# Performance work log

Hardware: AMD Instinct MI355X
Metric: run time of the kernel (lower is better)

The kernel has to match this reference:

```python
import jax, jax.numpy as jnp
import numpy as np

NH = 64
KS = 3
H_DIM = 32
IN_DIM = 1

# U-Net conv shapes, matching get_indices(unet_nh=64)
KERN_SHAPES = ([(NH, 2, KS, KS)] + [(NH, NH, KS, KS)] * 7
               + [(NH, 2 * NH, KS, KS), (NH, NH, KS, KS)] * 3
               + [(2, NH, 1, 1)])
BIAS_SHAPES = [(NH,)] * 14 + [(2,)]
KERN_SIZES = [int(np.prod(s)) for s in KERN_SHAPES]
BIAS_SIZES = [int(np.prod(s)) for s in BIAS_SHAPES]
OUT_DIM = sum(KERN_SIZES) + sum(BIAS_SIZES)  # 592002


def hypernet(hp, W1, b1, W2, b2, Wo, bo):
    # hp: [B, in_dim] -> per-sample flat weight vector [B, OUT_DIM]
    h = hp @ W1.T + b1          # no activation between lin1/lin2 (as in source)
    h = h @ W2.T + b2
    w = jnp.tanh(h @ Wo.T + bo)
    wl, bl = [], []
    off = 0
    for s, n in zip(KERN_SHAPES, KERN_SIZES):
        wl.append(w[:, off:off + n].reshape(-1, *s)); off += n
    for s, n in zip(BIAS_SHAPES, BIAS_SIZES):
        bl.append(w[:, off:off + n].reshape(-1, *s)); off += n
    return wl, bl, w


def bconv(x, w, b, pad):
    # per-sample conv: x [B,C,H,W], w [B,O,C,k,k], b [B,O]
    def one(xi, wi, bi):
        y = jax.lax.conv_general_dilated(xi[None], wi, (1, 1), [(pad, pad), (pad, pad)])
        return y[0] + bi[:, None, None]
    return jax.vmap(one)(x, w, b)


def maxpool2(x):
    B, C, H, W = x.shape
    return x.reshape(B, C, H // 2, 2, W // 2, 2).max(axis=(3, 5))


def up2_ac(x):
    # bilinear upsample scale=2, align_corners=True
    B, C, H, W = x.shape
    Ho, Wo = 2 * H, 2 * W
    ys = (jnp.arange(Ho, dtype=jnp.float32) * (H - 1) / (Ho - 1))
    y0 = jnp.floor(ys).astype(jnp.int32); y1 = jnp.minimum(y0 + 1, H - 1)
    wy = (ys - y0.astype(jnp.float32))[None, None, :, None]
    xs = (jnp.arange(Wo, dtype=jnp.float32) * (W - 1) / (Wo - 1))
    x0 = jnp.floor(xs).astype(jnp.int32); x1 = jnp.minimum(x0 + 1, W - 1)
    wx = (xs - x0.astype(jnp.float32))[None, None, None, :]
    r = x[:, :, y0, :] * (1 - wy) + x[:, :, y1, :] * wy
    return r[:, :, :, x0] * (1 - wx) + r[:, :, :, x1] * wx


def setup_inputs() -> dict:
    key = jax.random.key(0)
    ks = jax.random.split(key, 9)
    B, H, W = 8, 256, 256
    s1 = 1.0 / (IN_DIM * NH) ** 0.5
    s2 = 1.0 / (H_DIM * NH) ** 0.5
    return {
        "zf": jax.random.normal(ks[0], (B, H, W, 2), jnp.float32),
        "y": jax.random.normal(ks[1], (B, H, W, 2), jnp.float32),
        "hyperparams": jax.random.uniform(ks[2], (B, IN_DIM), jnp.float32),
        "W1": jax.random.normal(ks[3], (H_DIM, IN_DIM), jnp.float32) * s1,
        "b1": jax.random.normal(ks[4], (H_DIM,), jnp.float32) * s1,
        "W2": jax.random.normal(ks[5], (H_DIM, H_DIM), jnp.float32) * s2,
        "b2": jax.random.normal(ks[6], (H_DIM,), jnp.float32) * s2,
        "Wo": jax.random.normal(ks[7], (OUT_DIM, H_DIM), jnp.float32) * s2,
        "bo": jax.random.normal(ks[8], (OUT_DIM,), jnp.float32) * s2,
    }


def reference(zf, y, hyperparams, W1, b1, W2, b2, Wo, bo):
    wl, bl, flat = hypernet(hyperparams, W1, b1, W2, b2, Wo, bo)
    # l1 over all generated weights+biases == sum |flat| per sample
    l1_weights = jnp.sum(jnp.abs(flat), axis=1)
    relu = jax.nn.relu
    x = jnp.transpose(zf, (0, 3, 1, 2))  # [B,2,H,W]
    x = relu(bconv(x, wl[0], bl[0], 1))
    conv1 = relu(bconv(x, wl[1], bl[1], 1))
    x = maxpool2(conv1)
    x = relu(bconv(x, wl[2], bl[2], 1))
    conv2 = relu(bconv(x, wl[3], bl[3], 1))
    x = maxpool2(conv2)
    x = relu(bconv(x, wl[4], bl[4], 1))
    conv3 = relu(bconv(x, wl[5], bl[5], 1))
    x = maxpool2(conv3)
    x = relu(bconv(x, wl[6], bl[6], 1))
    conv4 = relu(bconv(x, wl[7], bl[7], 1))
    x = jnp.concatenate([up2_ac(conv4), conv3], axis=1)
    x = relu(bconv(x, wl[8], bl[8], 1))
    x = relu(bconv(x, wl[9], bl[9], 1))
    x = jnp.concatenate([up2_ac(x), conv2], axis=1)
    x = relu(bconv(x, wl[10], bl[10], 1))
    x = relu(bconv(x, wl[11], bl[11], 1))
    x = jnp.concatenate([up2_ac(x), conv1], axis=1)
    x = relu(bconv(x, wl[12], bl[12], 1))
    x = relu(bconv(x, wl[13], bl[13], 1))
    x = bconv(x, wl[14], bl[14], 0)  # 1x1 conv, padding=0
    x = jnp.transpose(x, (0, 2, 3, 1))
    x = zf + x  # residual=True
    return (x, l1_weights)
```

## Files before the change

kernel.cpp:

```cpp
#include <hip/hip_runtime.h>
#include <hip/hip_bf16.h>
#include <math.h>

#define ODIM 592002L
#define WRB  589824L
#define NB 8

typedef __hip_bfloat16 bf16;
typedef __bf16  bf16x8 __attribute__((ext_vector_type(8)));
typedef float   f32x16 __attribute__((ext_vector_type(16)));
typedef short   s16x8  __attribute__((ext_vector_type(8)));

__device__ __forceinline__ float b2f(bf16 x) { return __bfloat162float(x); }
__device__ __forceinline__ bf16 f2b(float x) { return __float2bfloat16(x); }
__device__ __forceinline__ bf16x8 bzero() { return __builtin_bit_cast(bf16x8, (s16x8)0); }

__global__ __launch_bounds__(256) void hyper_h(
    const float* __restrict__ hp, const float* __restrict__ W1,
    const float* __restrict__ b1, const float* __restrict__ W2,
    const float* __restrict__ b2, float* __restrict__ h2out)
{
    __shared__ float h1[NB][32];
    int t = threadIdx.x;
    int b = t >> 5, i = t & 31;
    h1[b][i] = hp[b] * W1[i] + b1[i];
    __syncthreads();
    float acc = b2[i];
    #pragma unroll
    for (int j = 0; j < 32; ++j) acc += h1[b][j] * W2[i * 32 + j];
    h2out[b * 32 + i] = acc;
}

__global__ __launch_bounds__(256) void genw(
    const float* __restrict__ Wo, const float* __restrict__ bo,
    const float* __restrict__ h2, bf16* __restrict__ wfb,
    float* __restrict__ part)
{
    __shared__ float h2s[256];
    __shared__ float red[256];
    int t = threadIdx.x;
    h2s[t] = h2[t];
    __syncthreads();
    long o = (long)blockIdx.x * 256 + t;
    float absacc[NB];
    #pragma unroll
    for (int b = 0; b < NB; ++b) absacc[b] = 0.f;
    if (o < ODIM) {
        float row[32];
        const float4* wp = (const float4*)(Wo + o * 32);
        #pragma unroll
        for (int q = 0; q < 8; ++q) {
            float4 v = wp[q];
            row[q*4+0] = v.x; row[q*4+1] = v.y; row[q*4+2] = v.z; row[q*4+3] = v.w;
        }
        float bias = bo[o];
        #pragma unroll
        for (int b = 0; b < NB; ++b) {
            float acc = bias;
            #pragma unroll
            for (int k = 0; k < 32; ++k) acc += h2s[b*32+k] * row[k];
            float w = tanhf(acc);
            wfb[(long)b * ODIM + o] = f2b(w);
            absacc[b] = fabsf(w);
        }
    }
    for (int b = 0; b < NB; ++b) {
        red[t] = absacc[b];
        __syncthreads();
        for (int s = 128; s > 0; s >>= 1) {
            if (t < s) red[t] += red[t + s];
            __syncthreads();
        }
        if (t == 0) part[(long)blockIdx.x * NB + b] = red[0];
        __syncthreads();
    }
}

__global__ __launch_bounds__(256) void l1_reduce(
    const float* __restrict__ part, int nblk, float* __restrict__ outp)
{
    __shared__ float red[256];
    int t = threadIdx.x; int b = t & 7, ch = t >> 3;
    float s = 0.f;
    for (int i = ch; i < nblk; i += 32) s += part[(long)i * 8 + b];
    red[t] = s;
    __syncthreads();
    for (int st = 128; st >= 8; st >>= 1) {
        if (t < st) red[t] += red[t + st];
        __syncthreads();
    }
    if (t < 8) outp[t] = red[t];
}

__global__ __launch_bounds__(256) void repack(
    const bf16* __restrict__ wfb, bf16* __restrict__ wr,
    int koff, int Cinfull, long roff, int K)
{
    int i = blockIdx.x * 256 + threadIdx.x;
    int b = blockIdx.y;
    if (i >= 64 * K) return;
    int fid = i >> 9;
    int lane = (i >> 3) & 63;
    int j = i & 7;
    int h = fid & 1;
    int kk = fid >> 1;
    int k4 = kk & 3;
    int tapq = kk >> 2;
    int tap = tapq % 9;
    int pass = tapq / 9;
    int oc = h * 32 + (lane & 31);
    int icf = pass * 64 + k4 * 16 + (lane >> 5) * 8 + j;
    wr[(long)b * WRB + roff + i] =
        wfb[(long)b * ODIM + koff + ((long)oc * Cinfull + icf) * 9 + tap];
}

template<int TR, int TC, int MODE>
__device__ __forceinline__ void stage_tile(
    const bf16* __restrict__ src, int Hc, int Wc, int y0, int x0,
    bf16* lin, int t)
{
    const int XL = TC + 2;
    const int total = (TR + 2) * XL * 8;
    for (int idx = t; idx < total; idx += 256) {
        const int g = idx & 7;
        const int rem = idx >> 3;
        const int xl = rem % XL;
        const int gy = y0 + rem / XL - 1, gx = x0 + xl - 1;
        bf16x8 v = bzero();
        if ((unsigned)gy < (unsigned)Hc && (unsigned)gx < (unsigned)Wc) {
            if constexpr (MODE == 0) {
                v = *(const bf16x8*)(src + (((long)gy * Wc) + gx) * 64 + g * 8);
            } else if constexpr (MODE == 1) {
                const int Ws = Wc * 2;
                const bf16* p = src + (((long)(gy*2) * Ws) + gx*2) * 64 + g * 8;
                bf16x8 aa = *(const bf16x8*)p;
                bf16x8 bb = *(const bf16x8*)(p + 64);
                bf16x8 cc = *(const bf16x8*)(p + (long)Ws * 64);
                bf16x8 dd = *(const bf16x8*)(p + (long)Ws * 64 + 64);
                #pragma unroll
                for (int j = 0; j < 8; ++j) {
                    float m = fmaxf(fmaxf((float)aa[j], (float)bb[j]),
                                    fmaxf((float)cc[j], (float)dd[j]));
                    v[j] = (__bf16)m;
                }
            } else {
                const int Hs = Hc >> 1, Ws = Wc >> 1;
                const float sy = (float)(Hs - 1) / (float)(Hc - 1);
                const float sx = (float)(Ws - 1) / (float)(Wc - 1);
                float ys = gy * sy, xs = gx * sx;
                int yy0 = (int)ys, xx0 = (int)xs;
                int yy1 = min(yy0 + 1, Hs - 1), xx1 = min(xx0 + 1, Ws - 1);
                float wy = ys - (float)yy0, wx = xs - (float)xx0;
                bf16x8 q00 = *(const bf16x8*)(src + ((long)yy0*Ws + xx0)*64 + g*8);
                bf16x8 q01 = *(const bf16x8*)(src + ((long)yy0*Ws + xx1)*64 + g*8);
                bf16x8 q10 = *(const bf16x8*)(src + ((long)yy1*Ws + xx0)*64 + g*8);
                bf16x8 q11 = *(const bf16x8*)(src + ((long)yy1*Ws + xx1)*64 + g*8);
                #pragma unroll
                for (int j = 0; j < 8; ++j) {
                    float r0 = (float)q00[j]*(1.f-wx) + (float)q01[j]*wx;
                    float r1 = (float)q10[j]*(1.f-wx) + (float)q11[j]*wx;
                    v[j] = (__bf16)(r0*(1.f-wy) + r1*wy);
                }
            }
        }
        long byte = (((long)rem) * 128 + g * 16) ^ ((xl & 7) << 4);
        *(bf16x8*)((char*)lin + byte) = v;
    }
}

template<int MODE>
__global__ __launch_bounds__(256, 3) void conv_mfma(
    const bf16* __restrict__ src1, const bf16* __restrict__ src2,
    int Hc, int Wc,
    const bf16* __restrict__ wr, long roff,
    const bf16* __restrict__ wfb, int boff,
    bf16* __restrict__ outp)
{
    const int TR = 8, TC = 32, XL = TC + 2;
    __shared__ bf16 lin[(TR + 2) * XL * 64];
    __shared__ float biasf[64];
    const int t = threadIdx.x;
    const int lane = t & 63;
    const int w = t >> 6;
    const int b = blockIdx.z;
    const int y0 = blockIdx.y * TR;
    const int x0 = blockIdx.x * TC;
    const int lx = lane & 31;

    f32x16 acc00 = {}, acc01 = {}, acc10 = {}, acc11 = {};

    const bf16* wl = wr + (long)b * WRB + roff;
    const long bb = (long)b * ODIM + boff;
    if (t < 64) biasf[t] = b2f(wfb[bb + t]);

    int xl128[3], swz[3];
    #pragma unroll
    for (int d = 0; d < 3; ++d) {
        int xl = lx + d;
        xl128[d] = xl * 128;
        swz[d] = (xl & 7) << 4;
    }
    const int icbl = (lane >> 5) * 16;

    auto kpass = [&](int p) {
        #pragma unroll
        for (int tap = 0; tap < 9; ++tap) {
            const int dy = tap / 3, dxi = tap % 3;
            const int rb0 = (w + dy) * (XL * 128);
            const int rb1 = (w + 4 + dy) * (XL * 128);
            bf16x8 af[4][2];
            #pragma unroll
            for (int k4 = 0; k4 < 4; ++k4) {
                const int fid = ((p * 9 + tap) * 4 + k4) * 2;
                const bf16* pk = wl + ((long)fid << 9) + (lane << 3);
                af[k4][0] = *(const bf16x8*)pk;
                af[k4][1] = *(const bf16x8*)(pk + 512);
            }
            #pragma unroll
            for (int k4 = 0; k4 < 4; ++k4) {
                const int co = xl128[dxi] + ((k4 * 32 + icbl) ^ swz[dxi]);
                bf16x8 b0 = *(const bf16x8*)((const char*)lin + rb0 + co);
                bf16x8 b1 = *(const bf16x8*)((const char*)lin + rb1 + co);
                acc00 = __builtin_amdgcn_mfma_f32_32x32x16_bf16(af[k4][0], b0, acc00, 0, 0, 0);
                acc01 = __builtin_amdgcn_mfma_f32_32x32x16_bf16(af[k4][1], b0, acc01, 0, 0, 0);
                acc10 = __builtin_amdgcn_mfma_f32_32x32x16_bf16(af[k4][0], b1, acc10, 0, 0, 0);
                acc11 = __builtin_amdgcn_mfma_f32_32x32x16_bf16(af[k4][1], b1, acc11, 0, 0, 0);
            }
        }
    };

    stage_tile<TR, TC, MODE>(src1, Hc, Wc, y0, x0, lin, t);
    __syncthreads();
    kpass(0);
    if (src2) {
        __syncthreads();
        stage_tile<TR, TC, 0>(src2, Hc, Wc, y0, x0, lin, t);
        __syncthreads();
        kpass(1);
    }

    __syncthreads();
    #pragma unroll
    for (int half = 0; half < 2; ++half) {
        const int r = w + half * 4;
        const int pixidx = r * TC + lx;
        const int psw = (pixidx & 7) << 4;
        #pragma unroll
        for (int ocs = 0; ocs < 2; ++ocs) {
            const f32x16& A = half ? (ocs ? acc11 : acc10) : (ocs ? acc01 : acc00);
            #pragma unroll
            for (int q = 0; q < 4; ++q) {
                const int oc0 = ocs * 32 + 8 * q + 4 * (lane >> 5);
                ushort4 pk;
                float v0 = fmaxf(A[4*q+0] + biasf[oc0 + 0], 0.f);
                float v1 = fmaxf(A[4*q+1] + biasf[oc0 + 1], 0.f);
                float v2 = fmaxf(A[4*q+2] + biasf[oc0 + 2], 0.f);
                float v3 = fmaxf(A[4*q+3] + biasf[oc0 + 3], 0.f);
                pk.x = __builtin_bit_cast(unsigned short, f2b(v0));
                pk.y = __builtin_bit_cast(unsigned short, f2b(v1));
                pk.z = __builtin_bit_cast(unsigned short, f2b(v2));
                pk.w = __builtin_bit_cast(unsigned short, f2b(v3));
                long byte = ((long)pixidx * 128 + oc0 * 2) ^ psw;
                *(ushort4*)((char*)lin + byte) = pk;
            }
        }
    }
    __syncthreads();
    bf16* outt = outp + (((long)b * Hc + y0) * Wc + x0) * 64;
    #pragma unroll
    for (int off = t * 16; off < TR * TC * 128; off += 4096) {
        int pix = off >> 7;
        int r = pix >> 5, c = pix & 31;
        long sb = (long)off ^ ((pix & 7) << 4);
        bf16x8 v = *(const bf16x8*)((const char*)lin + sb);
        *(bf16x8*)((char*)outt + ((long)(r * Wc + c)) * 128 + (off & 127)) = v;
    }
}

__global__ __launch_bounds__(256) void conv0_k(
    const float* __restrict__ zf, const bf16* __restrict__ wfb,
    bf16* __restrict__ outp)
{
    __shared__ float wsh[2][9][64];
    __shared__ float bsh[64];
    const int t = threadIdx.x;
    const int b = blockIdx.z;
    const long wb = (long)b * ODIM;
    for (int i = t; i < 1152; i += 256) {
        int oc = i / 18, r2 = i % 18, ic = r2 / 9, tap = r2 % 9;
        wsh[ic][tap][oc] = b2f(wfb[wb + i]);
    }
    if (t < 64) bsh[t] = b2f(wfb[wb + 591104 + t]);
    __syncthreads();
    const int pl = t >> 3, g = t & 7;
    const int pix = blockIdx.x * 32 + pl;
    const int y = pix >> 8, x = pix & 255;
    float acc[8];
    #pragma unroll
    for (int j = 0; j < 8; ++j) acc[j] = bsh[g * 8 + j];
    const float* zb = zf + (long)b * 131072;
    #pragma unroll
    for (int dy = 0; dy < 3; ++dy) {
        int yy = y + dy - 1;
        if ((unsigned)yy >= 256u) continue;
        #pragma unroll
        for (int dx = 0; dx < 3; ++dx) {
            int xx = x + dx - 1;
            if ((unsigned)xx >= 256u) continue;
            const float* p = zb + ((long)yy * 256 + xx) * 2;
            float v0 = p[0], v1 = p[1];
            int tap = dy * 3 + dx;
            #pragma unroll
            for (int j = 0; j < 8; ++j)
                acc[j] += v0 * wsh[0][tap][g*8+j] + v1 * wsh[1][tap][g*8+j];
        }
    }
    bf16x8 v;
    #pragma unroll
    for (int j = 0; j < 8; ++j) v[j] = (__bf16)fmaxf(acc[j], 0.f);
    *(bf16x8*)(outp + ((long)b * 65536 + pix) * 64 + g * 8) = v;
}

__global__ __launch_bounds__(256) void final_k(
    const bf16* __restrict__ X, const bf16* __restrict__ wfb,
    const float* __restrict__ zf, float* __restrict__ outp)
{
    __shared__ float wsh[128];
    __shared__ float bsh[2];
    const int t = threadIdx.x;
    const int i = blockIdx.x * 256 + t;
    const int pix = i & 65535;
    const int b = i >> 16;
    const long wb = (long)b * ODIM;
    if (t < 128) wsh[t] = b2f(wfb[wb + 590976 + t]);
    if (t < 2) bsh[t] = b2f(wfb[wb + 592000 + t]);
    __syncthreads();
    const bf16* p = X + ((long)b * 65536 + pix) * 64;
    float a0 = bsh[0], a1 = bsh[1];
    #pragma unroll
    for (int gq = 0; gq < 8; ++gq) {
        bf16x8 v = *(const bf16x8*)(p + gq * 8);
        #pragma unroll
        for (int j = 0; j < 8; ++j) {
            float f = (float)v[j];
            a0 += f * wsh[gq*8 + j];
            a1 += f * wsh[64 + gq*8 + j];
        }
    }
    long zi = ((long)b * 65536 + pix) * 2;
    outp[zi] = zf[zi] + a0;
    outp[zi + 1] = zf[zi + 1] + a1;
}

extern "C" void kernel_launch(void* const* d_in, const int* in_sizes, int n_in,
                              void* d_out, int out_size, void* d_ws, size_t ws_size,
                              hipStream_t stream)
{
    (void)in_sizes; (void)n_in; (void)out_size; (void)ws_size;
    const float* zf = (const float*)d_in[0];
    const float* hp = (const float*)d_in[2];
    const float* W1 = (const float*)d_in[3];
    const float* b1 = (const float*)d_in[4];
    const float* W2 = (const float*)d_in[5];
    const float* b2 = (const float*)d_in[6];
    const float* Wo = (const float*)d_in[7];
    const float* bo = (const float*)d_in[8];
    float* out = (float*)d_out;

    char* base = (char*)d_ws;
    float* h2   = (float*)base;  base += 1024;
    float* part = (float*)base;  base += 18504L * 4 + 32;
    bf16* wfb   = (bf16*)base;   base += 4736016L * 2 + 32;
    bf16* WREP  = (bf16*)base;   base += 4718592L * 2;
    bf16* Y256  = (bf16*)base;   base += 33554432L * 2;
    bf16* C1s   = (bf16*)base;   base += 33554432L * 2;
    bf16* D128a = (bf16*)base;   base += 8388608L * 2;
    bf16* C2s   = (bf16*)base;   base += 8388608L * 2;
    bf16* X128  = (bf16*)base;   base += 8388608L * 2;
    bf16* E64a  = (bf16*)base;   base += 2097152L * 2;
    bf16* C3s   = (bf16*)base;   base += 2097152L * 2;
    bf16* X64   = (bf16*)base;   base += 2097152L * 2;
    bf16* F32a  = (bf16*)base;   base += 524288L * 2;
    bf16* C4    = (bf16*)base;   base += 524288L * 2;

    hyper_h<<<1, 256, 0, stream>>>(hp, W1, b1, W2, b2, h2);
    const int ngb = (int)((ODIM + 255) / 256);
    genw<<<ngb, 256, 0, stream>>>(Wo, bo, h2, wfb, part);
    l1_reduce<<<1, 256, 0, stream>>>(part, ngb, out + 1048576);

    const int K1=1152, K2=38016, K3=74880, K4=111744, K5=148608,
              K6=185472, K7=222336, K8=259200, K9=332928, K10=369792,
              K11=443520, K12=480384, K13=554112;
    const int BB = 591104;
    const long R1=0, R2=36864, R3=73728, R4=110592, R5=147456, R6=184320,
               R7=221184, R8=258048, R9=331776, R10=368640, R11=442368,
               R12=479232, R13=552960;

    repack<<<dim3(144, 8), 256, 0, stream>>>(wfb, WREP, K1, 64, R1, 576);
    repack<<<dim3(144, 8), 256, 0, stream>>>(wfb, WREP, K2, 64, R2, 576);
    repack<<<dim3(144, 8), 256, 0, stream>>>(wfb, WREP, K3, 64, R3, 576);
    repack<<<dim3(144, 8), 256, 0, stream>>>(wfb, WREP, K4, 64, R4, 576);
    repack<<<dim3(144, 8), 256, 0, stream>>>(wfb, WREP, K5, 64, R5, 576);
    repack<<<dim3(144, 8), 256, 0, stream>>>(wfb, WREP, K6, 64, R6, 576);
    repack<<<dim3(144, 8), 256, 0, stream>>>(wfb, WREP, K7, 64, R7, 576);
    repack<<<dim3(288, 8), 256, 0, stream>>>(wfb, WREP, K8, 128, R8, 1152);
    repack<<<dim3(144, 8), 256, 0, stream>>>(wfb, WREP, K9, 64, R9, 576);
    repack<<<dim3(288, 8), 256, 0, stream>>>(wfb, WREP, K10, 128, R10, 1152);
    repack<<<dim3(144, 8), 256, 0, stream>>>(wfb, WREP, K11, 64, R11, 576);
    repack<<<dim3(288, 8), 256, 0, stream>>>(wfb, WREP, K12, 128, R12, 1152);
    repack<<<dim3(144, 8), 256, 0, stream>>>(wfb, WREP, K13, 64, R13, 576);

    conv0_k<<<dim3(2048, 1, 8), 256, 0, stream>>>(zf, wfb, Y256);

    conv_mfma<0><<<dim3(8,32,8),  256, 0, stream>>>(Y256, nullptr, 256,256, WREP, R1,  wfb, BB+64,  C1s);
    conv_mfma<1><<<dim3(4,16,8),  256, 0, stream>>>(C1s,  nullptr, 128,128, WREP, R2,  wfb, BB+128, D128a);
    conv_mfma<0><<<dim3(4,16,8),  256, 0, stream>>>(D128a,nullptr, 128,128, WREP, R3,  wfb, BB+192, C2s);
    conv_mfma<1><<<dim3(2,8,8),   256, 0, stream>>>(C2s,  nullptr, 64,64,   WREP, R4,  wfb, BB+256, E64a);
    conv_mfma<0><<<dim3(2,8,8),   256, 0, stream>>>(E64a, nullptr, 64,64,   WREP, R5,  wfb, BB+320, C3s);
    conv_mfma<1><<<dim3(1,4,8),   256, 0, stream>>>(C3s,  nullptr, 32,32,   WREP, R6,  wfb, BB+384, F32a);
    conv_mfma<0><<<dim3(1,4,8),   256, 0, stream>>>(F32a, nullptr, 32,32,   WREP, R7,  wfb, BB+448, C4);
    conv_mfma<2><<<dim3(2,8,8),   256, 0, stream>>>(C4,   C3s, 64,64,   WREP, R8,  wfb, BB+512, E64a);
    conv_mfma<0><<<dim3(2,8,8),   256, 0, stream>>>(E64a, nullptr, 64,64, WREP, R9,  wfb, BB+576, X64);
    conv_mfma<2><<<dim3(4,16,8),  256, 0, stream>>>(X64,  C2s, 128,128, WREP, R10, wfb, BB+640, D128a);
    conv_mfma<0><<<dim3(4,16,8),  256, 0, stream>>>(D128a,nullptr,128,128, WREP, R11, wfb, BB+704, X128);
    conv_mfma<2><<<dim3(8,32,8),  256, 0, stream>>>(X128, C1s, 256,256, WREP, R12, wfb, BB+768, Y256);
    conv_mfma<0><<<dim3(8,32,8),  256, 0, stream>>>(Y256, nullptr,256,256, WREP, R13, wfb, BB+832, C1s);

    final_k<<<dim3(2048), 256, 0, stream>>>(C1s, wfb, zf, out);
}
```

Baseline: 629.7 us.

## Enlarge conv tiles to 16 rows with register row reuse; merge repack launches

The MFMA conv kernel now processes 16-row tiles. Each wave owns 4 consecutive output rows and keeps 6 input rows of LDS fragments in registers, so the three dy taps reuse loaded B fragments and each weight fragment feeds 8 MFMAs instead of 4. Occupancy in launch bounds drops from 3 to 2 blocks per CU to fit the larger accumulator and fragment state, and the grids are halved, which leaves fewer blocks on the small layers. The 13 weight-repack launches are merged into one kernel that selects each layer's offsets by index range.

```diff
diff --git a/kernel.cpp b/kernel.cpp
--- a/kernel.cpp
+++ b/kernel.cpp
@@ -92,16 +92,32 @@
     if (t < 8) outp[t] = red[t];
 }
 
-__global__ __launch_bounds__(256) void repack(
-    const bf16* __restrict__ wfb, bf16* __restrict__ wr,
-    int koff, int Cinfull, long roff, int K)
+__global__ __launch_bounds__(256) void repack_all(
+    const bf16* __restrict__ wfb, bf16* __restrict__ wr)
 {
     int i = blockIdx.x * 256 + threadIdx.x;
     int b = blockIdx.y;
-    if (i >= 64 * K) return;
-    int fid = i >> 9;
-    int lane = (i >> 3) & 63;
-    int j = i & 7;
+    if (i >= (int)WRB) return;
+    int roff, koff, dual = 0;
+    if      (i < 36864)  { roff = 0;      koff = 1152;  }
+    else if (i < 73728)  { roff = 36864;  koff = 38016; }
+    else if (i < 110592) { roff = 73728;  koff = 74880; }
+    else if (i < 147456) { roff = 110592; koff = 111744;}
+    else if (i < 184320) { roff = 147456; koff = 148608;}
+    else if (i < 221184) { roff = 184320; koff = 185472;}
+    else if (i < 258048) { roff = 221184; koff = 222336;}
+    else if (i < 331776) { roff = 258048; koff = 259200; dual = 1; }
+    else if (i < 368640) { roff = 331776; koff = 332928;}
+    else if (i < 442368) { roff = 368640; koff = 369792; dual = 1; }
+    else if (i < 479232) { roff = 442368; koff = 443520;}
+    else if (i < 552960) { roff = 479232; koff = 480384; dual = 1; }
+    else                 { roff = 552960; koff = 554112;}
+    int li = i - roff;
+    int K = dual ? 1152 : 576;
+    int Cinfull = dual ? 128 : 64;
+    int fid = li >> 9;
+    int lane = (li >> 3) & 63;
+    int j = li & 7;
     int h = fid & 1;
     int kk = fid >> 1;
     int k4 = kk & 3;
@@ -110,7 +126,8 @@
     int pass = tapq / 9;
     int oc = h * 32 + (lane & 31);
     int icf = pass * 64 + k4 * 16 + (lane >> 5) * 8 + j;
-    wr[(long)b * WRB + roff + i] =
+    (void)K;
+    wr[(long)b * WRB + i] =
         wfb[(long)b * ODIM + koff + ((long)oc * Cinfull + icf) * 9 + tap];
 }
 
@@ -169,14 +186,14 @@
 }
 
 template<int MODE>
-__global__ __launch_bounds__(256, 3) void conv_mfma(
+__global__ __launch_bounds__(256, 2) void conv_mfma(
     const bf16* __restrict__ src1, const bf16* __restrict__ src2,
     int Hc, int Wc,
     const bf16* __restrict__ wr, long roff,
     const bf16* __restrict__ wfb, int boff,
     bf16* __restrict__ outp)
 {
-    const int TR = 8, TC = 32, XL = TC + 2;
+    const int TR = 16, TC = 32, XL = TC + 2;
     __shared__ bf16 lin[(TR + 2) * XL * 64];
     __shared__ float biasf[64];
     const int t = threadIdx.x;
@@ -187,44 +204,59 @@
     const int x0 = blockIdx.x * TC;
     const int lx = lane & 31;
 
-    f32x16 acc00 = {}, acc01 = {}, acc10 = {}, acc11 = {};
+    f32x16 acc[4][2];
+    #pragma unroll
+    for (int r = 0; r < 4; ++r) {
+        acc[r][0] = {}; acc[r][1] = {};
+    }
 
     const bf16* wl = wr + (long)b * WRB + roff;
-    const long bb = (long)b * ODIM + boff;
-    if (t < 64) biasf[t] = b2f(wfb[bb + t]);
-
-    int xl128[3], swz[3];
+    if (t < 64) biasf[t] = b2f(wfb[(long)b * ODIM + boff + t]);
+
+    int cofs[3], swz[3];
     #pragma unroll
     for (int d = 0; d < 3; ++d) {
         int xl = lx + d;
-        xl128[d] = xl * 128;
+        cofs[d] = xl * 128;
         swz[d] = (xl & 7) << 4;
     }
     const int icbl = (lane >> 5) * 16;
+    const int wrow = 4 * w;
 
     auto kpass = [&](int p) {
         #pragma unroll
-        for (int tap = 0; tap < 9; ++tap) {
-            const int dy = tap / 3, dxi = tap % 3;
-            const int rb0 = (w + dy) * (XL * 128);
-            const int rb1 = (w + 4 + dy) * (XL * 128);
-            bf16x8 af[4][2];
+        for (int k4 = 0; k4 < 4; ++k4) {
+            const int cb = k4 * 32 + icbl;
+            bf16x8 bf[6][3];
             #pragma unroll
-            for (int k4 = 0; k4 < 4; ++k4) {
-                const int fid = ((p * 9 + tap) * 4 + k4) * 2;
-                const bf16* pk = wl + ((long)fid << 9) + (lane << 3);
-                af[k4][0] = *(const bf16x8*)pk;
-                af[k4][1] = *(const bf16x8*)(pk + 512);
+            for (int rr = 0; rr < 4; ++rr) {
+                const int rb = (wrow + rr) * (XL * 128);
+                #pragma unroll
+                for (int d = 0; d < 3; ++d)
+                    bf[rr][d] = *(const bf16x8*)((const char*)lin + rb + cofs[d] + (cb ^ swz[d]));
             }
             #pragma unroll
-            for (int k4 = 0; k4 < 4; ++k4) {
-                const int co = xl128[dxi] + ((k4 * 32 + icbl) ^ swz[dxi]);
-                bf16x8 b0 = *(const bf16x8*)((const char*)lin + rb0 + co);
-                bf16x8 b1 = *(const bf16x8*)((const char*)lin + rb1 + co);
-                acc00 = __builtin_amdgcn_mfma_f32_32x32x16_bf16(af[k4][0], b0, acc00, 0, 0, 0);
-                acc01 = __builtin_amdgcn_mfma_f32_32x32x16_bf16(af[k4][1], b0, acc01, 0, 0, 0);
-                acc10 = __builtin_amdgcn_mfma_f32_32x32x16_bf16(af[k4][0], b1, acc10, 0, 0, 0);
-                acc11 = __builtin_amdgcn_mfma_f32_32x32x16_bf16(af[k4][1], b1, acc11, 0, 0, 0);
+            for (int dy = 0; dy < 3; ++dy) {
+                if (dy) {
+                    const int rr = dy + 3;
+                    const int rb = (wrow + rr) * (XL * 128);
+                    #pragma unroll
+                    for (int d = 0; d < 3; ++d)
+                        bf[rr][d] = *(const bf16x8*)((const char*)lin + rb + cofs[d] + (cb ^ swz[d]));
+                }
+                #pragma unroll
+                for (int dxi = 0; dxi < 3; ++dxi) {
+                    const int tap = dy * 3 + dxi;
+                    const int fid = ((p * 9 + tap) * 4 + k4) * 2;
+                    const bf16* pk = wl + ((long)fid << 9) + (lane << 3);
+                    bf16x8 a0 = *(const bf16x8*)pk;
+                    bf16x8 a1 = *(const bf16x8*)(pk + 512);
+                    #pragma unroll
+                    for (int r = 0; r < 4; ++r) {
+                        acc[r][0] = __builtin_amdgcn_mfma_f32_32x32x16_bf16(a0, bf[r + dy][dxi], acc[r][0], 0, 0, 0);
+                        acc[r][1] = __builtin_amdgcn_mfma_f32_32x32x16_bf16(a1, bf[r + dy][dxi], acc[r][1], 0, 0, 0);
+                    }
+                }
             }
         }
     };
@@ -241,13 +273,12 @@
 
     __syncthreads();
     #pragma unroll
-    for (int half = 0; half < 2; ++half) {
-        const int r = w + half * 4;
-        const int pixidx = r * TC + lx;
+    for (int r = 0; r < 4; ++r) {
+        const int pixidx = (wrow + r) * TC + lx;
         const int psw = (pixidx & 7) << 4;
         #pragma unroll
         for (int ocs = 0; ocs < 2; ++ocs) {
-            const f32x16& A = half ? (ocs ? acc11 : acc10) : (ocs ? acc01 : acc00);
+            const f32x16& A = acc[r][ocs];
             #pragma unroll
             for (int q = 0; q < 4; ++q) {
                 const int oc0 = ocs * 32 + 8 * q + 4 * (lane >> 5);
@@ -388,43 +419,28 @@
     genw<<<ngb, 256, 0, stream>>>(Wo, bo, h2, wfb, part);
     l1_reduce<<<1, 256, 0, stream>>>(part, ngb, out + 1048576);
 
-    const int K1=1152, K2=38016, K3=74880, K4=111744, K5=148608,
-              K6=185472, K7=222336, K8=259200, K9=332928, K10=369792,
-              K11=443520, K12=480384, K13=554112;
     const int BB = 591104;
     const long R1=0, R2=36864, R3=73728, R4=110592, R5=147456, R6=184320,
                R7=221184, R8=258048, R9=331776, R10=368640, R11=442368,
                R12=479232, R13=552960;
 
-    repack<<<dim3(144, 8), 256, 0, stream>>>(wfb, WREP, K1, 64, R1, 576);
-    repack<<<dim3(144, 8), 256, 0, stream>>>(wfb, WREP, K2, 64, R2, 576);
-    repack<<<dim3(144, 8), 256, 0, stream>>>(wfb, WREP, K3, 64, R3, 576);
-    repack<<<dim3(144, 8), 256, 0, stream>>>(wfb, WREP, K4, 64, R4, 576);
-    repack<<<dim3(144, 8), 256, 0, stream>>>(wfb, WREP, K5, 64, R5, 576);
-    repack<<<dim3(144, 8), 256, 0, stream>>>(wfb, WREP, K6, 64, R6, 576);
-    repack<<<dim3(144, 8), 256, 0, stream>>>(wfb, WREP, K7, 64, R7, 576);
-    repack<<<dim3(288, 8), 256, 0, stream>>>(wfb, WREP, K8, 128, R8, 1152);
-    repack<<<dim3(144, 8), 256, 0, stream>>>(wfb, WREP, K9, 64, R9, 576);
-    repack<<<dim3(288, 8), 256, 0, stream>>>(wfb, WREP, K10, 128, R10, 1152);
-    repack<<<dim3(144, 8), 256, 0, stream>>>(wfb, WREP, K11, 64, R11, 576);
-    repack<<<dim3(288, 8), 256, 0, stream>>>(wfb, WREP, K12, 128, R12, 1152);
-    repack<<<dim3(144, 8), 256, 0, stream>>>(wfb, WREP, K13, 64, R13, 576);
+    repack_all<<<dim3(2304, 8), 256, 0, stream>>>(wfb, WREP);
 
     conv0_k<<<dim3(2048, 1, 8), 256, 0, stream>>>(zf, wfb, Y256);
 
-    conv_mfma<0><<<dim3(8,32,8),  256, 0, stream>>>(Y256, nullptr, 256,256, WREP, R1,  wfb, BB+64,  C1s);
-    conv_mfma<1><<<dim3(4,16,8),  256, 0, stream>>>(C1s,  nullptr, 128,128, WREP, R2,  wfb, BB+128, D128a);
-    conv_mfma<0><<<dim3(4,16,8),  256, 0, stream>>>(D128a,nullptr, 128,128, WREP, R3,  wfb, BB+192, C2s);
-    conv_mfma<1><<<dim3(2,8,8),   256, 0, stream>>>(C2s,  nullptr, 64,64,   WREP, R4,  wfb, BB+256, E64a);
-    conv_mfma<0><<<dim3(2,8,8),   256, 0, stream>>>(E64a, nullptr, 64,64,   WREP, R5,  wfb, BB+320, C3s);
-    conv_mfma<1><<<dim3(1,4,8),   256, 0, stream>>>(C3s,  nullptr, 32,32,   WREP, R6,  wfb, BB+384, F32a);
-    conv_mfma<0><<<dim3(1,4,8),   256, 0, stream>>>(F32a, nullptr, 32,32,   WREP, R7,  wfb, BB+448, C4);
-    conv_mfma<2><<<dim3(2,8,8),   256, 0, stream>>>(C4,   C3s, 64,64,   WREP, R8,  wfb, BB+512, E64a);
-    conv_mfma<0><<<dim3(2,8,8),   256, 0, stream>>>(E64a, nullptr, 64,64, WREP, R9,  wfb, BB+576, X64);
-    conv_mfma<2><<<dim3(4,16,8),  256, 0, stream>>>(X64,  C2s, 128,128, WREP, R10, wfb, BB+640, D128a);
-    conv_mfma<0><<<dim3(4,16,8),  256, 0, stream>>>(D128a,nullptr,128,128, WREP, R11, wfb, BB+704, X128);
-    conv_mfma<2><<<dim3(8,32,8),  256, 0, stream>>>(X128, C1s, 256,256, WREP, R12, wfb, BB+768, Y256);
-    conv_mfma<0><<<dim3(8,32,8),  256, 0, stream>>>(Y256, nullptr,256,256, WREP, R13, wfb, BB+832, C1s);
+    conv_mfma<0><<<dim3(8,16,8),  256, 0, stream>>>(Y256, nullptr, 256,256, WREP, R1,  wfb, BB+64,  C1s);
+    conv_mfma<1><<<dim3(4,8,8),   256, 0, stream>>>(C1s,  nullptr, 128,128, WREP, R2,  wfb, BB+128, D128a);
+    conv_mfma<0><<<dim3(4,8,8),   256, 0, stream>>>(D128a,nullptr, 128,128, WREP, R3,  wfb, BB+192, C2s);
+    conv_mfma<1><<<dim3(2,4,8),   256, 0, stream>>>(C2s,  nullptr, 64,64,   WREP, R4,  wfb, BB+256, E64a);
+    conv_mfma<0><<<dim3(2,4,8),   256, 0, stream>>>(E64a, nullptr, 64,64,   WREP, R5,  wfb, BB+320, C3s);
+    conv_mfma<1><<<dim3(1,2,8),   256, 0, stream>>>(C3s,  nullptr, 32,32,   WREP, R6,  wfb, BB+384, F32a);
+    conv_mfma<0><<<dim3(1,2,8),   256, 0, stream>>>(F32a, nullptr, 32,32,   WREP, R7,  wfb, BB+448, C4);
+    conv_mfma<2><<<dim3(2,4,8),   256, 0, stream>>>(C4,   C3s, 64,64,   WREP, R8,  wfb, BB+512, E64a);
+    conv_mfma<0><<<dim3(2,4,8),   256, 0, stream>>>(E64a, nullptr, 64,64, WREP, R9,  wfb, BB+576, X64);
+    conv_mfma<2><<<dim3(4,8,8),   256, 0, stream>>>(X64,  C2s, 128,128, WREP, R10, wfb, BB+640, D128a);
+    conv_mfma<0><<<dim3(4,8,8),   256, 0, stream>>>(D128a,nullptr,128,128, WREP, R11, wfb, BB+704, X128);
+    conv_mfma<2><<<dim3(8,16,8),  256, 0, stream>>>(X128, C1s, 256,256, WREP, R12, wfb, BB+768, Y256);
+    conv_mfma<0><<<dim3(8,16,8),  256, 0, stream>>>(Y256, nullptr,256,256, WREP, R13, wfb, BB+832, C1s);
 
     final_k<<<dim3(2048), 256, 0, stream>>>(C1s, wfb, zf, out);
 }
```

Result: slower. 714.2 us (+13.4%).
